# Performance work log

Measured on AMD Instinct MI355X. Metric: run time of the kernel, lower is better.

The kernel has to match this reference:

```python
import jax, jax.numpy as jnp
import numpy as np

D = 1024      # hidden_size
FF = 4096     # ff_inner_dim = 4 * D
E = 8         # num_experts
K = 2         # moe_top_k
B, L = 4, 1024


def setup_inputs() -> dict:
    key = jax.random.key(0)
    ks = jax.random.split(key, 12)
    s = 0.02  # weight init scale
    return {
        "x": jax.random.normal(ks[0], (B, L, D), jnp.float32),
        "W_gate": jax.random.normal(ks[1], (D, E), jnp.float32) * s,
        "W1": jax.random.normal(ks[2], (E, D, FF), jnp.float32) * s,
        "b1": jnp.zeros((E, FF), jnp.float32),
        "W2": jax.random.normal(ks[3], (E, FF, D), jnp.float32) * s,
        "b2": jnp.zeros((E, D), jnp.float32),
        "Ws1": jax.random.normal(ks[4], (D, FF), jnp.float32) * s,
        "bs1": jnp.zeros((FF,), jnp.float32),
        "Ws2": jax.random.normal(ks[5], (FF, D), jnp.float32) * s,
        "bs2": jnp.zeros((D,), jnp.float32),
    }


def _gelu(h):
    # torch F.gelu default = exact (erf) gelu
    return jax.nn.gelu(h, approximate=False)


def reference(x, W_gate, W1, b1, W2, b2, Ws1, bs1, Ws2, bs2):
    Bx, Lx, Dx = x.shape
    xf = x.reshape(-1, Dx)                       # [T, D]
    logits = xf @ W_gate                         # [T, E]
    probs = jax.nn.softmax(logits, axis=-1)
    top_v, top_i = jax.lax.top_k(probs, K)       # [T, K]
    top_v = top_v / jnp.sum(top_v, axis=-1, keepdims=True)
    # dense combine weights: [T, E], zero for unselected experts
    combine = jnp.sum(jax.nn.one_hot(top_i, E, dtype=xf.dtype) * top_v[..., None], axis=1)

    out = jnp.zeros_like(xf)
    for e in range(E):  # fixed small expert loop, unrolled under jit
        h = _gelu(xf @ W1[e] + b1[e])            # [T, FF]
        out = out + combine[:, e:e + 1] * (h @ W2[e] + b2[e])

    shared = _gelu(xf @ Ws1 + bs1) @ Ws2 + bs2   # [T, D]
    return (out + shared).reshape(Bx, Lx, Dx)
```

## Files before the change

### kernel.cpp

```cpp
#include <hip/hip_runtime.h>
#include <hip/hip_bf16.h>

typedef unsigned short ushort_t;
typedef __attribute__((ext_vector_type(4))) float f32x4;
typedef __attribute__((ext_vector_type(8))) short bf16x8;
typedef __attribute__((ext_vector_type(8))) unsigned short us8;

#define T_TOK 4096
#define D_DIM 1024
#define FF_DIM 4096
#define NE 8
#define ESTRIDE 4194304L

__device__ __forceinline__ unsigned short f2bf(float f) {
  __hip_bfloat16 h = __float2bfloat16(f);
  return __builtin_bit_cast(unsigned short, h);
}
__device__ __forceinline__ float gelu_f(float v) {
  return 0.5f * v * (1.0f + erff(v * 0.70710678118654752440f));
}

__global__ void gate_kernel(const float* __restrict__ x, const float* __restrict__ Wg,
                            int* __restrict__ cnt, int* __restrict__ tok,
                            float* __restrict__ wof, int* __restrict__ rankof) {
  const int t = blockIdx.x;
  const int lane = threadIdx.x;
  const float* xr = x + (long)t * D_DIM;
  float acc[NE];
#pragma unroll
  for (int e = 0; e < NE; e++) acc[e] = 0.f;
#pragma unroll
  for (int i = 0; i < 16; i++) {
    int d = i * 64 + lane;
    float xv = xr[d];
    const float* wr = Wg + d * NE;
#pragma unroll
    for (int e = 0; e < NE; e++) acc[e] += xv * wr[e];
  }
#pragma unroll
  for (int off = 32; off > 0; off >>= 1) {
#pragma unroll
    for (int e = 0; e < NE; e++) acc[e] += __shfl_xor(acc[e], off, 64);
  }
  if (lane == 0) {
    int i0 = 0;
#pragma unroll
    for (int e = 1; e < NE; e++) if (acc[e] > acc[i0]) i0 = e;
    int i1 = -1;
#pragma unroll
    for (int e = 0; e < NE; e++) {
      if (e == i0) continue;
      if (i1 < 0 || acc[e] > acc[i1]) i1 = e;
    }
    float e1 = expf(acc[i1] - acc[i0]);
    float w0 = 1.f / (1.f + e1);
    float w1 = e1 * w0;
    int s0 = atomicAdd(&cnt[i0], 1);
    tok[i0 * T_TOK + s0] = t; wof[i0 * T_TOK + s0] = w0; rankof[i0 * T_TOK + s0] = 0;
    int s1 = atomicAdd(&cnt[i1], 1);
    tok[i1 * T_TOK + s1] = t; wof[i1 * T_TOK + s1] = w1; rankof[i1 * T_TOK + s1] = 1;
    tok[8 * T_TOK + t] = t; wof[8 * T_TOK + t] = 1.f; rankof[8 * T_TOK + t] = 0;
  }
}

__global__ void scan_kernel(int* cnt, int* base) {
  if (threadIdx.x == 0 && blockIdx.x == 0) {
    int s = 0;
    for (int e = 0; e < NE; e++) { base[e] = s; s += cnt[e]; }
    base[8] = s;
    cnt[8] = T_TOK;
  }
}

__global__ void cvt_x_kernel(const float* __restrict__ src, ushort_t* __restrict__ dst) {
  long i = ((long)blockIdx.x * 256 + threadIdx.x) * 8;
  float4 v0 = *(const float4*)(src + i);
  float4 v1 = *(const float4*)(src + i + 4);
  us8 o;
  o[0] = f2bf(v0.x); o[1] = f2bf(v0.y); o[2] = f2bf(v0.z); o[3] = f2bf(v0.w);
  o[4] = f2bf(v1.x); o[5] = f2bf(v1.y); o[6] = f2bf(v1.z); o[7] = f2bf(v1.w);
  *(us8*)(dst + i) = o;
}

__global__ void tcvt_kernel(const float* __restrict__ src, ushort_t* __restrict__ dst,
                            int R, int C) {
  src += (long)blockIdx.z * R * C;
  dst += (long)blockIdx.z * R * C;
  const int r0 = blockIdx.y * 64, c0 = blockIdx.x * 64;
  __shared__ ushort_t tile[64][72];
  const int t = threadIdx.x;
#pragma unroll
  for (int i = 0; i < 4; i++) {
    int lin = t + i * 256;
    int r = lin >> 4;
    int c = (lin & 15) * 4;
    float4 v = *(const float4*)(src + (long)(r0 + r) * C + c0 + c);
    tile[c + 0][r] = f2bf(v.x);
    tile[c + 1][r] = f2bf(v.y);
    tile[c + 2][r] = f2bf(v.z);
    tile[c + 3][r] = f2bf(v.w);
  }
  __syncthreads();
#pragma unroll
  for (int i = 0; i < 2; i++) {
    int lin = t + i * 256;
    int cc = lin >> 3, rp = lin & 7;
    us8 v = *(const us8*)&tile[cc][rp * 8];
    *(us8*)(dst + (long)(c0 + cc) * R + r0 + rp * 8) = v;
  }
}

template <int K, int N, int PHASE>
__global__ __launch_bounds__(256, 2) void gemm_kernel(
    const ushort_t* __restrict__ Abase, const ushort_t* __restrict__ WT,
    const float* __restrict__ bias_e, const float* __restrict__ bias_s,
    const int* __restrict__ cnt, const int* __restrict__ base,
    const int* __restrict__ tok, const float* __restrict__ wof,
    const int* __restrict__ rankof,
    ushort_t* __restrict__ He, float* __restrict__ ybuf, float* __restrict__ out) {
  const int e = blockIdx.z;
  const int count = cnt[e];
  const int m0 = blockIdx.y * 128;
  if (m0 >= count) return;
  const int n0 = blockIdx.x * 128;
  const int tid = threadIdx.x;
  const int w = tid >> 6, lane = tid & 63;

  __shared__ ushort_t sA[128 * 32];
  __shared__ ushort_t sB[128 * 32];

  const ushort_t* pA[2];
  const ushort_t* pB[2];
#pragma unroll
  for (int j = 0; j < 2; j++) {
    int c = w * 128 + j * 64 + lane;
    int r = c >> 2, kp = c & 3;
    int rr = m0 + r;
    int rc = (rr < count) ? rr : 0;
    long arow;
    if (PHASE == 1) arow = tok[e * T_TOK + rc];
    else            arow = (long)base[e] + rc;
    pA[j] = Abase + arow * K + kp * 8;
    pB[j] = WT + (long)e * ESTRIDE + (long)(n0 + r) * K + kp * 8;
  }

  f32x4 acc[4][4] = {};
  const int wm = w >> 1, wn = w & 1;
  const int lr = lane & 15, lg = lane >> 4;
  const int lds0 = (w * 128) * 16;
  const int lds1 = (w * 128 + 64) * 16;

  for (int k0 = 0; k0 < K; k0 += 32) {
    __builtin_amdgcn_global_load_lds(
        (const __attribute__((address_space(1))) void*)(pA[0] + k0),
        (__attribute__((address_space(3))) void*)((char*)sA + lds0), 16, 0, 0);
    __builtin_amdgcn_global_load_lds(
        (const __attribute__((address_space(1))) void*)(pA[1] + k0),
        (__attribute__((address_space(3))) void*)((char*)sA + lds1), 16, 0, 0);
    __builtin_amdgcn_global_load_lds(
        (const __attribute__((address_space(1))) void*)(pB[0] + k0),
        (__attribute__((address_space(3))) void*)((char*)sB + lds0), 16, 0, 0);
    __builtin_amdgcn_global_load_lds(
        (const __attribute__((address_space(1))) void*)(pB[1] + k0),
        (__attribute__((address_space(3))) void*)((char*)sB + lds1), 16, 0, 0);
    __syncthreads();

    bf16x8 av[4], bv[4];
#pragma unroll
    for (int m = 0; m < 4; m++)
      av[m] = *(const bf16x8*)&sA[(wm * 64 + m * 16 + lr) * 32 + lg * 8];
#pragma unroll
    for (int n = 0; n < 4; n++)
      bv[n] = *(const bf16x8*)&sB[(wn * 64 + n * 16 + lr) * 32 + lg * 8];
#pragma unroll
    for (int m = 0; m < 4; m++)
#pragma unroll
      for (int n = 0; n < 4; n++)
        acc[m][n] = __builtin_amdgcn_mfma_f32_16x16x32_bf16(av[m], bv[n], acc[m][n], 0, 0, 0);
    __syncthreads();
  }

  const float* bias = (e == NE) ? bias_s : (bias_e + (long)e * N);
#pragma unroll
  for (int m = 0; m < 4; m++) {
#pragma unroll
    for (int j = 0; j < 4; j++) {
      int rloc = wm * 64 + m * 16 + lg * 4 + j;
      int rr = m0 + rloc;
      if (rr >= count) continue;
      if (PHASE == 1) {
        long orow = (long)base[e] + rr;
#pragma unroll
        for (int n = 0; n < 4; n++) {
          int col = n0 + wn * 64 + n * 16 + lr;
          float v = acc[m][n][j] + bias[col];
          He[orow * FF_DIM + col] = f2bf(gelu_f(v));
        }
      } else {
        int tt = tok[e * T_TOK + rr];
        if (e == NE) {
#pragma unroll
          for (int n = 0; n < 4; n++) {
            int col = n0 + wn * 64 + n * 16 + lr;
            out[(long)tt * D_DIM + col] = acc[m][n][j] + bias[col];
          }
        } else {
          float wgt = wof[e * T_TOK + rr];
          int rk = rankof[e * T_TOK + rr];
          float* dst = ybuf + (long)rk * ((long)T_TOK * D_DIM) + (long)tt * D_DIM;
#pragma unroll
          for (int n = 0; n < 4; n++) {
            int col = n0 + wn * 64 + n * 16 + lr;
            dst[col] = wgt * (acc[m][n][j] + bias[col]);
          }
        }
      }
    }
  }
}

__global__ void final_add_kernel(float* __restrict__ out, const float* __restrict__ ybuf) {
  long i = ((long)blockIdx.x * 256 + threadIdx.x) * 4;
  float4 a = *(const float4*)(out + i);
  float4 b = *(const float4*)(ybuf + i);
  float4 c = *(const float4*)(ybuf + (long)T_TOK * D_DIM + i);
  a.x += b.x + c.x; a.y += b.y + c.y; a.z += b.z + c.z; a.w += b.w + c.w;
  *(float4*)(out + i) = a;
}

extern "C" void kernel_launch(void* const* d_in, const int* in_sizes, int n_in,
                              void* d_out, int out_size, void* d_ws, size_t ws_size,
                              hipStream_t stream) {
  (void)in_sizes; (void)n_in; (void)out_size; (void)ws_size;
  const float* x   = (const float*)d_in[0];
  const float* Wg  = (const float*)d_in[1];
  const float* W1  = (const float*)d_in[2];
  const float* b1  = (const float*)d_in[3];
  const float* W2  = (const float*)d_in[4];
  const float* b2  = (const float*)d_in[5];
  const float* Ws1 = (const float*)d_in[6];
  const float* bs1 = (const float*)d_in[7];
  const float* Ws2 = (const float*)d_in[8];
  const float* bs2 = (const float*)d_in[9];
  float* out = (float*)d_out;

  char* ws = (char*)d_ws;
  int*      cnt    = (int*)(ws + 0);
  int*      base   = (int*)(ws + 64);
  int*      tok    = (int*)(ws + 256);
  float*    wof    = (float*)(ws + 256 + 147456);
  int*      rankof = (int*)(ws + 256 + 2 * 147456);
  ushort_t* Xbf    = (ushort_t*)(ws + 442624);
  ushort_t* W1T    = (ushort_t*)(ws + 8831232);
  ushort_t* Ws1T   = W1T + 8L * ESTRIDE;
  ushort_t* W2T    = (ushort_t*)(ws + 84328704);
  ushort_t* Ws2T   = W2T + 8L * ESTRIDE;
  ushort_t* He     = (ushort_t*)(ws + 159826176);
  float*    ybuf   = (float*)(ws + 261538048);
  (void)Ws1T; (void)Ws2T;

  hipMemsetAsync(cnt, 0, 64, stream);
  gate_kernel<<<T_TOK, 64, 0, stream>>>(x, Wg, cnt, tok, wof, rankof);
  scan_kernel<<<1, 64, 0, stream>>>(cnt, base);
  cvt_x_kernel<<<2048, 256, 0, stream>>>(x, Xbf);
  tcvt_kernel<<<dim3(64, 16, 8), 256, 0, stream>>>(W1, W1T, 1024, 4096);
  tcvt_kernel<<<dim3(16, 64, 8), 256, 0, stream>>>(W2, W2T, 4096, 1024);
  tcvt_kernel<<<dim3(64, 16, 1), 256, 0, stream>>>(Ws1, W1T + 8L * ESTRIDE, 1024, 4096);
  tcvt_kernel<<<dim3(16, 64, 1), 256, 0, stream>>>(Ws2, W2T + 8L * ESTRIDE, 4096, 1024);
  gemm_kernel<1024, 4096, 1><<<dim3(32, 32, 9), 256, 0, stream>>>(
      Xbf, W1T, b1, bs1, cnt, base, tok, wof, rankof, He, ybuf, out);
  gemm_kernel<4096, 1024, 2><<<dim3(8, 32, 9), 256, 0, stream>>>(
      He, W2T, b2, bs2, cnt, base, tok, wof, rankof, He, ybuf, out);
  final_add_kernel<<<4096, 256, 0, stream>>>(out, ybuf);
}
```

Baseline: 585.1 us.

## Double-buffer LDS tiles in MoE GEMM and raise launch-bounds occupancy

Splits the LDS A/B tiles into two buffers so the global-to-LDS loads for the next K slice are issued before the MFMA work on the current slice, overlapping memory latency with compute. It also raises the launch-bounds minimum blocks per SM from 2 to 4, which constrains registers per thread. The 64-float accumulator plus fragment registers may spill under the tighter register limit. The doubled LDS (32KB per block) also limits how many blocks fit on a CU.

```diff
diff --git a/kernel.cpp b/kernel.cpp
--- a/kernel.cpp
+++ b/kernel.cpp
@@ -111,7 +111,7 @@
 }
 
 template <int K, int N, int PHASE>
-__global__ __launch_bounds__(256, 2) void gemm_kernel(
+__global__ __launch_bounds__(256, 4) void gemm_kernel(
     const ushort_t* __restrict__ Abase, const ushort_t* __restrict__ WT,
     const float* __restrict__ bias_e, const float* __restrict__ bias_s,
     const int* __restrict__ cnt, const int* __restrict__ base,
@@ -126,8 +126,8 @@
   const int tid = threadIdx.x;
   const int w = tid >> 6, lane = tid & 63;
 
-  __shared__ ushort_t sA[128 * 32];
-  __shared__ ushort_t sB[128 * 32];
+  __shared__ ushort_t sA[2 * 128 * 32];
+  __shared__ ushort_t sB[2 * 128 * 32];
 
   const ushort_t* pA[2];
   const ushort_t* pB[2];
@@ -144,41 +144,57 @@
     pB[j] = WT + (long)e * ESTRIDE + (long)(n0 + r) * K + kp * 8;
   }
 
+  const int lds0 = (w * 128) * 16;
+  const int lds1 = (w * 128 + 64) * 16;
+
+#define STAGE4(buf, kk)                                                                \
+  do {                                                                                 \
+    char* dA = (char*)sA + (buf) * 8192;                                               \
+    char* dB = (char*)sB + (buf) * 8192;                                               \
+    __builtin_amdgcn_global_load_lds(                                                  \
+        (const __attribute__((address_space(1))) void*)(pA[0] + (kk)),                 \
+        (__attribute__((address_space(3))) void*)(dA + lds0), 16, 0, 0);               \
+    __builtin_amdgcn_global_load_lds(                                                  \
+        (const __attribute__((address_space(1))) void*)(pA[1] + (kk)),                 \
+        (__attribute__((address_space(3))) void*)(dA + lds1), 16, 0, 0);               \
+    __builtin_amdgcn_global_load_lds(                                                  \
+        (const __attribute__((address_space(1))) void*)(pB[0] + (kk)),                 \
+        (__attribute__((address_space(3))) void*)(dB + lds0), 16, 0, 0);               \
+    __builtin_amdgcn_global_load_lds(                                                  \
+        (const __attribute__((address_space(1))) void*)(pB[1] + (kk)),                 \
+        (__attribute__((address_space(3))) void*)(dB + lds1), 16, 0, 0);               \
+  } while (0)
+
   f32x4 acc[4][4] = {};
   const int wm = w >> 1, wn = w & 1;
   const int lr = lane & 15, lg = lane >> 4;
-  const int lds0 = (w * 128) * 16;
-  const int lds1 = (w * 128 + 64) * 16;
-
+
+  STAGE4(0, 0);
+  __syncthreads();
+
+  int cur = 0;
   for (int k0 = 0; k0 < K; k0 += 32) {
-    __builtin_amdgcn_global_load_lds(
-        (const __attribute__((address_space(1))) void*)(pA[0] + k0),
-        (__attribute__((address_space(3))) void*)((char*)sA + lds0), 16, 0, 0);
-    __builtin_amdgcn_global_load_lds(
-        (const __attribute__((address_space(1))) void*)(pA[1] + k0),
-        (__attribute__((address_space(3))) void*)((char*)sA + lds1), 16, 0, 0);
-    __builtin_amdgcn_global_load_lds(
-        (const __attribute__((address_space(1))) void*)(pB[0] + k0),
-        (__attribute__((address_space(3))) void*)((char*)sB + lds0), 16, 0, 0);
-    __builtin_amdgcn_global_load_lds(
-        (const __attribute__((address_space(1))) void*)(pB[1] + k0),
-        (__attribute__((address_space(3))) void*)((char*)sB + lds1), 16, 0, 0);
-    __syncthreads();
-
+    if (k0 + 32 < K) STAGE4(cur ^ 1, k0 + 32);
+
+    const ushort_t* sAc = sA + cur * 4096;
+    const ushort_t* sBc = sB + cur * 4096;
     bf16x8 av[4], bv[4];
 #pragma unroll
     for (int m = 0; m < 4; m++)
-      av[m] = *(const bf16x8*)&sA[(wm * 64 + m * 16 + lr) * 32 + lg * 8];
+      av[m] = *(const bf16x8*)&sAc[(wm * 64 + m * 16 + lr) * 32 + lg * 8];
 #pragma unroll
     for (int n = 0; n < 4; n++)
-      bv[n] = *(const bf16x8*)&sB[(wn * 64 + n * 16 + lr) * 32 + lg * 8];
+      bv[n] = *(const bf16x8*)&sBc[(wn * 64 + n * 16 + lr) * 32 + lg * 8];
 #pragma unroll
     for (int m = 0; m < 4; m++)
 #pragma unroll
       for (int n = 0; n < 4; n++)
         acc[m][n] = __builtin_amdgcn_mfma_f32_16x16x32_bf16(av[m], bv[n], acc[m][n], 0, 0, 0);
+
     __syncthreads();
-  }
+    cur ^= 1;
+  }
+#undef STAGE4
 
   const float* bias = (e == NE) ? bias_s : (bias_e + (long)e * N);
 #pragma unroll
@@ -252,12 +268,9 @@
   int*      rankof = (int*)(ws + 256 + 2 * 147456);
   ushort_t* Xbf    = (ushort_t*)(ws + 442624);
   ushort_t* W1T    = (ushort_t*)(ws + 8831232);
-  ushort_t* Ws1T   = W1T + 8L * ESTRIDE;
   ushort_t* W2T    = (ushort_t*)(ws + 84328704);
-  ushort_t* Ws2T   = W2T + 8L * ESTRIDE;
   ushort_t* He     = (ushort_t*)(ws + 159826176);
   float*    ybuf   = (float*)(ws + 261538048);
-  (void)Ws1T; (void)Ws2T;
 
   hipMemsetAsync(cnt, 0, 64, stream);
   gate_kernel<<<T_TOK, 64, 0, stream>>>(x, Wg, cnt, tok, wof, rankof);
```

After: 595.3 us. Within noise of the previous version (+1.7%).

## Rewrite expert GEMM as 256x256 tile, 8-wave, 4-stage LDS pipelined kernel

Applied to the files above, without the earlier changes.

Replaces the 128x128, 4-wave single-buffered GEMM with a 256x256 tile on 512 threads. A 16-slot LDS ring streams global_load_lds two K-steps ahead, with vmcnt-based waits in place of the two barriers per step. LDS reads use an XOR swizzle to avoid bank conflicts, and s_setprio is raised around the MFMA bursts. The larger tiles raise arithmetic intensity and latency hiding, but use 128KB of LDS, which limits occupancy. They also cause more padding waste for experts with small token counts.

```diff
diff --git a/kernel.cpp b/kernel.cpp
--- a/kernel.cpp
+++ b/kernel.cpp
@@ -111,7 +111,7 @@
 }
 
 template <int K, int N, int PHASE>
-__global__ __launch_bounds__(256, 2) void gemm_kernel(
+__global__ __launch_bounds__(512, 2) void gemm_kernel(
     const ushort_t* __restrict__ Abase, const ushort_t* __restrict__ WT,
     const float* __restrict__ bias_e, const float* __restrict__ bias_s,
     const int* __restrict__ cnt, const int* __restrict__ base,
@@ -120,72 +120,108 @@
     ushort_t* __restrict__ He, float* __restrict__ ybuf, float* __restrict__ out) {
   const int e = blockIdx.z;
   const int count = cnt[e];
-  const int m0 = blockIdx.y * 128;
+  const int m0 = blockIdx.y * 256;
   if (m0 >= count) return;
-  const int n0 = blockIdx.x * 128;
+  const int n0 = blockIdx.x * 256;
   const int tid = threadIdx.x;
   const int w = tid >> 6, lane = tid & 63;
-
-  __shared__ ushort_t sA[128 * 32];
-  __shared__ ushort_t sB[128 * 32];
-
-  const ushort_t* pA[2];
-  const ushort_t* pB[2];
-#pragma unroll
-  for (int j = 0; j < 2; j++) {
-    int c = w * 128 + j * 64 + lane;
-    int r = c >> 2, kp = c & 3;
-    int rr = m0 + r;
+  const int wm = w >> 2, wn = w & 3;
+  const int lr = lane & 15, lg = lane >> 4;
+
+  __shared__ ushort_t lds_u[16 * 4096];
+  char* const lds = (char*)lds_u;
+
+  constexpr int NT = K / 32;
+
+  const int srow = tid >> 2;
+  const int kcg = (tid & 3) ^ ((tid >> 3) & 3);
+  const ushort_t* bsrc[4];
+#pragma unroll
+  for (int c = 0; c < 2; c++) {
+    int rr = m0 + c * 128 + srow;
     int rc = (rr < count) ? rr : 0;
     long arow;
     if (PHASE == 1) arow = tok[e * T_TOK + rc];
     else            arow = (long)base[e] + rc;
-    pA[j] = Abase + arow * K + kp * 8;
-    pB[j] = WT + (long)e * ESTRIDE + (long)(n0 + r) * K + kp * 8;
-  }
-
-  f32x4 acc[4][4] = {};
-  const int wm = w >> 1, wn = w & 1;
-  const int lr = lane & 15, lg = lane >> 4;
-  const int lds0 = (w * 128) * 16;
-  const int lds1 = (w * 128 + 64) * 16;
-
-  for (int k0 = 0; k0 < K; k0 += 32) {
-    __builtin_amdgcn_global_load_lds(
-        (const __attribute__((address_space(1))) void*)(pA[0] + k0),
-        (__attribute__((address_space(3))) void*)((char*)sA + lds0), 16, 0, 0);
-    __builtin_amdgcn_global_load_lds(
-        (const __attribute__((address_space(1))) void*)(pA[1] + k0),
-        (__attribute__((address_space(3))) void*)((char*)sA + lds1), 16, 0, 0);
-    __builtin_amdgcn_global_load_lds(
-        (const __attribute__((address_space(1))) void*)(pB[0] + k0),
-        (__attribute__((address_space(3))) void*)((char*)sB + lds0), 16, 0, 0);
-    __builtin_amdgcn_global_load_lds(
-        (const __attribute__((address_space(1))) void*)(pB[1] + k0),
-        (__attribute__((address_space(3))) void*)((char*)sB + lds1), 16, 0, 0);
-    __syncthreads();
-
-    bf16x8 av[4], bv[4];
-#pragma unroll
-    for (int m = 0; m < 4; m++)
-      av[m] = *(const bf16x8*)&sA[(wm * 64 + m * 16 + lr) * 32 + lg * 8];
-#pragma unroll
-    for (int n = 0; n < 4; n++)
-      bv[n] = *(const bf16x8*)&sB[(wn * 64 + n * 16 + lr) * 32 + lg * 8];
-#pragma unroll
-    for (int m = 0; m < 4; m++)
-#pragma unroll
-      for (int n = 0; n < 4; n++)
-        acc[m][n] = __builtin_amdgcn_mfma_f32_16x16x32_bf16(av[m], bv[n], acc[m][n], 0, 0, 0);
-    __syncthreads();
-  }
+    bsrc[c] = Abase + arow * (long)K + kcg * 8;
+  }
+#pragma unroll
+  for (int c = 0; c < 2; c++) {
+    long brow = n0 + c * 128 + srow;
+    bsrc[2 + c] = WT + (long)e * ESTRIDE + brow * (long)K + kcg * 8;
+  }
+
+#define STAGE(g_, c_, tg_)                                                     \
+  __builtin_amdgcn_global_load_lds(                                            \
+      (const __attribute__((address_space(1))) void*)(bsrc[c_] + (long)(tg_) * 32), \
+      (__attribute__((address_space(3))) void*)(lds + ((g_) & 15) * 8192 + w * 1024), \
+      16, 0, 0)
+
+  int offA[8], offB[4];
+#pragma unroll
+  for (int m = 0; m < 8; m++) {
+    int r = m * 16 + lr;
+    offA[m] = r * 64 + ((lg ^ ((r >> 1) & 3)) << 4);
+  }
+#pragma unroll
+  for (int n = 0; n < 4; n++) {
+    int r = (wn & 1) * 64 + n * 16 + lr;
+    offB[n] = r * 64 + ((lg ^ ((r >> 1) & 3)) << 4);
+  }
+
+  f32x4 acc[8][4] = {};
+
+#pragma unroll
+  for (int g = 0; g < 8; g++) STAGE(g, g & 3, g >> 2);
+
+  int sA = wm;
+  int sB = 2 + (wn >> 1);
+
+  for (int t = 0; t < NT; t++) {
+    if (t == NT - 1) { asm volatile("s_waitcnt vmcnt(0)" ::: "memory"); }
+    else             { asm volatile("s_waitcnt vmcnt(4)" ::: "memory"); }
+    __builtin_amdgcn_s_barrier();
+    asm volatile("" ::: "memory");
+
+    const char* pa = lds + sA * 8192;
+    const char* pb = lds + sB * 8192;
+
+    if (t + 2 < NT) { STAGE(4 * t + 8, 0, t + 2); STAGE(4 * t + 9, 1, t + 2); }
+    bf16x8 av[8];
+#pragma unroll
+    for (int m = 0; m < 8; m++) av[m] = *(const bf16x8*)(pa + offA[m]);
+    bf16x8 bv0 = *(const bf16x8*)(pb + offB[0]);
+    bf16x8 bv1 = *(const bf16x8*)(pb + offB[1]);
+    __builtin_amdgcn_s_setprio(1);
+#pragma unroll
+    for (int m = 0; m < 8; m++) {
+      acc[m][0] = __builtin_amdgcn_mfma_f32_16x16x32_bf16(av[m], bv0, acc[m][0], 0, 0, 0);
+      acc[m][1] = __builtin_amdgcn_mfma_f32_16x16x32_bf16(av[m], bv1, acc[m][1], 0, 0, 0);
+    }
+    __builtin_amdgcn_s_setprio(0);
+
+    if (t + 2 < NT) { STAGE(4 * t + 10, 2, t + 2); STAGE(4 * t + 11, 3, t + 2); }
+    bf16x8 bv2 = *(const bf16x8*)(pb + offB[2]);
+    bf16x8 bv3 = *(const bf16x8*)(pb + offB[3]);
+    __builtin_amdgcn_s_setprio(1);
+#pragma unroll
+    for (int m = 0; m < 8; m++) {
+      acc[m][2] = __builtin_amdgcn_mfma_f32_16x16x32_bf16(av[m], bv2, acc[m][2], 0, 0, 0);
+      acc[m][3] = __builtin_amdgcn_mfma_f32_16x16x32_bf16(av[m], bv3, acc[m][3], 0, 0, 0);
+    }
+    __builtin_amdgcn_s_setprio(0);
+
+    sA = (sA + 4) & 15;
+    sB = (sB + 4) & 15;
+  }
+#undef STAGE
 
   const float* bias = (e == NE) ? bias_s : (bias_e + (long)e * N);
 #pragma unroll
-  for (int m = 0; m < 4; m++) {
+  for (int m = 0; m < 8; m++) {
 #pragma unroll
     for (int j = 0; j < 4; j++) {
-      int rloc = wm * 64 + m * 16 + lg * 4 + j;
+      int rloc = wm * 128 + m * 16 + lg * 4 + j;
       int rr = m0 + rloc;
       if (rr >= count) continue;
       if (PHASE == 1) {
@@ -252,12 +288,9 @@
   int*      rankof = (int*)(ws + 256 + 2 * 147456);
   ushort_t* Xbf    = (ushort_t*)(ws + 442624);
   ushort_t* W1T    = (ushort_t*)(ws + 8831232);
-  ushort_t* Ws1T   = W1T + 8L * ESTRIDE;
   ushort_t* W2T    = (ushort_t*)(ws + 84328704);
-  ushort_t* Ws2T   = W2T + 8L * ESTRIDE;
   ushort_t* He     = (ushort_t*)(ws + 159826176);
   float*    ybuf   = (float*)(ws + 261538048);
-  (void)Ws1T; (void)Ws2T;
 
   hipMemsetAsync(cnt, 0, 64, stream);
   gate_kernel<<<T_TOK, 64, 0, stream>>>(x, Wg, cnt, tok, wof, rankof);
@@ -267,9 +300,9 @@
   tcvt_kernel<<<dim3(16, 64, 8), 256, 0, stream>>>(W2, W2T, 4096, 1024);
   tcvt_kernel<<<dim3(64, 16, 1), 256, 0, stream>>>(Ws1, W1T + 8L * ESTRIDE, 1024, 4096);
   tcvt_kernel<<<dim3(16, 64, 1), 256, 0, stream>>>(Ws2, W2T + 8L * ESTRIDE, 4096, 1024);
-  gemm_kernel<1024, 4096, 1><<<dim3(32, 32, 9), 256, 0, stream>>>(
+  gemm_kernel<1024, 4096, 1><<<dim3(16, 16, 9), 512, 0, stream>>>(
       Xbf, W1T, b1, bs1, cnt, base, tok, wof, rankof, He, ybuf, out);
-  gemm_kernel<4096, 1024, 2><<<dim3(8, 32, 9), 256, 0, stream>>>(
+  gemm_kernel<4096, 1024, 2><<<dim3(4, 16, 9), 512, 0, stream>>>(
       He, W2T, b2, bs2, cnt, base, tok, wof, rankof, He, ybuf, out);
   final_add_kernel<<<4096, 256, 0, stream>>>(out, ybuf);
 }
```

Result: slower. 627.3 us (+7.2%).
